# Performance work log

Hardware: AMD Instinct MI355X
Metric: run time of the kernel (lower is better)

Reference implementation:

```python
import jax, jax.numpy as jnp
import numpy as np

P = 7    # output_size (7,7)
SR = 2   # sampling_ratio per bin (torchvision roi_align samples per bin)


def _roi_avg_pool(feature_map, rois):
    """Fused roi_align(output_size=PxP) + adaptive_avg_pool2d(1,1).

    Since every bin averages SR*SR equally-weighted samples and the global
    average pool then averages the P*P bins, the result equals the mean over
    all P*SR x P*SR bilinear samples -- the 7x7 grid is never materialized.
    """
    B, C, H, W = feature_map.shape
    bidx = rois[:, 0].astype(jnp.int32)                       # [N]
    # get_anns: fp32 math, stored into an fp16 tensor (replicate the rounding).
    # NOTE (faithful to source): x coords are scaled by H (shape[2]) and y by W.
    f16 = lambda v: v.astype(jnp.float16).astype(jnp.float32)
    x1 = f16((rois[:, 2] - 0.5 * rois[:, 4]) * H)
    y1 = f16((rois[:, 3] - 0.5 * rois[:, 5]) * W)
    x2 = f16((rois[:, 2] + 0.5 * rois[:, 4]) * H)
    y2 = f16((rois[:, 3] + 0.5 * rois[:, 5]) * W)

    # torchvision roi_align, spatial_scale=1, aligned=False
    roi_w = jnp.maximum(x2 - x1, 1.0)
    roi_h = jnp.maximum(y2 - y1, 1.0)
    # sample offsets: bin pw plus (ix+0.5)/SR within the bin, in units of bin size
    offs = (jnp.arange(P, dtype=jnp.float32)[:, None]
            + (jnp.arange(SR, dtype=jnp.float32)[None, :] + 0.5) / SR).reshape(-1)  # [P*SR]
    xs = x1[:, None] + offs[None, :] * (roi_w / P)[:, None]   # [N,S] along width
    ys = y1[:, None] + offs[None, :] * (roi_h / P)[:, None]   # [N,S] along height

    valid = (((ys > -1.0) & (ys < H))[:, :, None]
             & ((xs > -1.0) & (xs < W))[:, None, :])          # [N,S,S]
    yc = jnp.clip(ys, 0.0, H - 1.0)
    xc = jnp.clip(xs, 0.0, W - 1.0)
    y0 = jnp.floor(yc).astype(jnp.int32)
    x0 = jnp.floor(xc).astype(jnp.int32)
    y1i = jnp.minimum(y0 + 1, H - 1)
    x1i = jnp.minimum(x0 + 1, W - 1)
    ly = yc - y0
    lx = xc - x0
    hy = 1.0 - ly
    hx = 1.0 - lx

    feat_t = jnp.transpose(feature_map, (0, 2, 3, 1))         # [B,H,W,C]

    def gather(yy, xx):  # yy,xx: [N,S] -> [N,S,S,C]
        return feat_t[bidx[:, None, None], yy[:, :, None], xx[:, None, :]]

    w = lambda a, b: (a[:, :, None] * b[:, None, :])[..., None]
    val = (w(hy, hx) * gather(y0, x0) + w(hy, lx) * gather(y0, x1i)
           + w(ly, hx) * gather(y1i, x0) + w(ly, lx) * gather(y1i, x1i))
    val = jnp.where(valid[..., None], val, 0.0)
    return val.mean(axis=(1, 2))                              # [N,C]


def setup_inputs() -> dict:
    key = jax.random.key(0)
    k1, k2, k3, k4 = jax.random.split(key, 4)
    B, C, H, W, N = 4, 256, 128, 128, 512
    feature_map = jax.random.normal(k1, (B, C, H, W), dtype=jnp.float32)
    # sorted batch indices so the original per-batch regrouping keeps ROI order
    bidx = jnp.sort(jax.random.randint(k2, (N,), 0, B)).astype(jnp.float32)
    cls = jax.random.randint(k3, (N,), 0, 20).astype(jnp.float32)
    kc, kw = jax.random.split(k4)
    cxcy = jax.random.uniform(kc, (N, 2), minval=0.2, maxval=0.8, dtype=jnp.float32)
    wh = jax.random.uniform(kw, (N, 2), minval=0.05, maxval=0.4, dtype=jnp.float32)
    rois = jnp.concatenate([bidx[:, None], cls[:, None], cxcy, wh], axis=1)  # [N,6]
    return {"feature_map": feature_map, "rois": rois}


def reference(feature_map, rois):
    roi_feats = _roi_avg_pool(feature_map, rois)   # [N, C] (original returns len-N list of [1,C])
    gt = rois[:, 1]                                # class labels
    return roi_feats, gt
```

## Files before the change

### kernel.cpp

```cpp
#include <hip/hip_runtime.h>
#include <hip/hip_fp16.h>
#include <hip/hip_bf16.h>

#define PP 7
#define SR 2
#define HH 128
#define WW 128
#define CC 256
#define PLANE (HH * WW)
#define MAXB 8
#define SLOT_BYTES 32768
#define WY_BASE (8 * SLOT_BYTES)
#define TAB_OFF (2 * WY_BASE)

typedef unsigned int uint;
typedef short bf16x8 __attribute__((ext_vector_type(8)));
typedef float f32x16 __attribute__((ext_vector_type(16)));

typedef const __attribute__((address_space(1))) void g_void;
typedef __attribute__((address_space(3))) void l_void;

__device__ __forceinline__ void gload_lds16(const void* g, void* lds_base) {
  __builtin_amdgcn_global_load_lds((g_void*)g, (l_void*)lds_base, 16, 0, 0);
}

__device__ __forceinline__ uint pkbf(float a, float b) {
  __hip_bfloat16 ha = __float2bfloat16(a), hb = __float2bfloat16(b);
  return (uint)*(unsigned short*)&ha | ((uint)*(unsigned short*)&hb << 16);
}

__global__ __launch_bounds__(64) void setup_kernel(
    const float* __restrict__ rois, unsigned char* wsb, int N, int B) {
  __shared__ int c[MAXB];
  const int t = threadIdx.x;
  if (t < MAXB) c[t] = 0;
  __syncthreads();
  for (int j = t; j < N; j += 64) atomicAdd(&c[(int)rois[j * 6]], 1);
  __syncthreads();
  if (t == 0) {
    int* tab = (int*)(wsb + TAB_OFF);
    int s = 0, tb = 0;
    for (int i = 0; i < B; ++i) {
      tab[i] = s; tab[24 + i] = c[i];
      const int tc = (c[i] + 127) >> 7;
      tab[8 + i] = tc; tab[16 + i] = tb;
      s += c[i]; tb += tc;
    }
  }
}

__global__ __launch_bounds__(64) void roi_meta_kernel(
    const float* __restrict__ rois, unsigned char* wsb,
    float* __restrict__ out, int N) {
  const int roi = blockIdx.x;
  const int lane = threadIdx.x;

  __shared__ float WXs[WW], WYs[HH];
  WXs[lane] = 0.f; WXs[lane + 64] = 0.f;
  WYs[lane] = 0.f; WYs[lane + 64] = 0.f;
  __syncthreads();

  const float bf = rois[roi * 6 + 0];
  const float cx = rois[roi * 6 + 2];
  const float cy = rois[roi * 6 + 3];
  const float w_ = rois[roi * 6 + 4];
  const float h_ = rois[roi * 6 + 5];

  const float x1 = __half2float(__float2half(
      __fmul_rn(__fsub_rn(cx, __fmul_rn(0.5f, w_)), 128.0f)));
  const float y1 = __half2float(__float2half(
      __fmul_rn(__fsub_rn(cy, __fmul_rn(0.5f, h_)), 128.0f)));
  const float x2 = __half2float(__float2half(
      __fmul_rn(__fadd_rn(cx, __fmul_rn(0.5f, w_)), 128.0f)));
  const float y2 = __half2float(__float2half(
      __fmul_rn(__fadd_rn(cy, __fmul_rn(0.5f, h_)), 128.0f)));

  const float sx = fmaxf(__fsub_rn(x2, x1), 1.0f) / 7.0f;
  const float sy = fmaxf(__fsub_rn(y2, y1), 1.0f) / 7.0f;

  if (lane < 2 * PP * SR) {
    const int isX = lane >= PP * SR;
    const int i = lane - isX * PP * SR;
    const float off = (float)(i >> 1) + ((float)(i & 1) + 0.5f) * 0.5f;
    const float pos = __fadd_rn(isX ? x1 : y1, __fmul_rn(off, isX ? sx : sy));
    if (pos > -1.0f && pos < 128.0f) {
      const float pc = fminf(fmaxf(pos, 0.0f), 127.0f);
      const int p0 = (int)floorf(pc);
      const int p1 = min(p0 + 1, 127);
      const float l = pc - (float)p0;
      float* Warr = isX ? WXs : WYs;
      atomicAdd(&Warr[p0], 1.0f - l);
      atomicAdd(&Warr[p1], l);
    }
  }
  __syncthreads();

  const int* tab = (const int*)(wsb + TAB_OFF);
  const int img = (int)bf;
  const int rl = roi - tab[img];
  const int slot = tab[16 + img] + (rl >> 7);
  const int col = rl & 127;

  const int sw = ((((lane >> 2) ^ (col & 7)) << 4) | ((lane & 3) << 2));
  *(uint*)(wsb + (size_t)slot * SLOT_BYTES + col * 256 + sw) =
      pkbf(WXs[2 * lane], WXs[2 * lane + 1]);
  __hip_bfloat16 h0 = __float2bfloat16(WYs[lane]);
  __hip_bfloat16 h1 = __float2bfloat16(WYs[lane + 64]);
  unsigned char* wyb = wsb + WY_BASE + (size_t)slot * SLOT_BYTES + col * 2;
  *(unsigned short*)(wyb + lane * 256) = *(unsigned short*)&h0;
  *(unsigned short*)(wyb + (lane + 64) * 256) = *(unsigned short*)&h1;

  if (lane == 0) out[(size_t)N * CC + roi] = rois[roi * 6 + 1];
}

__global__ __launch_bounds__(256, 2) void roi_gemm_kernel(
    const float* __restrict__ fm, const unsigned char* __restrict__ wsb,
    float* __restrict__ out, int N) {
  const int bid = blockIdx.x;
  const int ch = bid & (CC - 1);
  const int img = bid >> 8;
  const int t = threadIdx.x, wave = t >> 6, lane = t & 63;

  const int* tab = (const int*)(wsb + TAB_OFF);
  const int tcnt = tab[8 + img];
  if (tcnt == 0) return;
  const int istart = tab[img], Rimg = tab[24 + img], tbase = tab[16 + img];

  __shared__ unsigned char A[32768];
  __shared__ unsigned char BXl[32768];
  __shared__ float partial[4][128];

  const float* pb = fm + ((size_t)img * CC + ch) * PLANE;
  #pragma unroll
  for (int k = 0; k < 8; ++k) {
    const int cid = k * 256 + t;
    const float4 v0 = *(const float4*)(pb + (size_t)cid * 8);
    const float4 v1 = *(const float4*)(pb + (size_t)cid * 8 + 4);
    const int row = cid >> 4, x8 = cid & 15;
    const int boff = (row << 8) | ((x8 ^ (row & 7)) << 4);
    uint4 u;
    u.x = pkbf(v0.x, v0.y); u.y = pkbf(v0.z, v0.w);
    u.z = pkbf(v1.x, v1.y); u.w = pkbf(v1.z, v1.w);
    *(uint4*)(A + boff) = u;
  }

  const int m0 = wave * 32;
  const int arow = m0 + (lane & 31);
  const int ar7 = arow & 7;
  const unsigned char* Arow = A + (arow << 8);
  const int ahalf = lane >> 5;
  const int r7 = lane & 7;

  for (int ti = 0; ti < tcnt; ++ti) {
    const unsigned char* BXg = wsb + (size_t)(tbase + ti) * SLOT_BYTES;
    const unsigned char* BY = wsb + WY_BASE + (size_t)(tbase + ti) * SLOT_BYTES;

    #pragma unroll
    for (int k2 = 0; k2 < 8; ++k2)
      gload_lds16(BXg + k2 * 4096 + wave * 1024 + (lane << 4),
                  BXl + k2 * 4096 + wave * 1024);
    asm volatile("s_waitcnt vmcnt(0)" ::: "memory");
    __syncthreads();

    f32x16 ac0 = {}, ac1 = {}, ac2 = {}, ac3 = {};

    auto ldA = [&](int ks) -> bf16x8 {
      const int idx = (ahalf + 2 * ks) ^ ar7;
      return *(const bf16x8*)(Arow + (idx << 4));
    };
    auto ldB = [&](int ks, int ni) -> bf16x8 {
      const int c = (2 * ks + ahalf) ^ r7;
      return *(const bf16x8*)(BXl + (((lane & 31) + 32 * ni) << 8) + (c << 4));
    };

    bf16x8 a = ldA(0);
    bf16x8 b0 = ldB(0, 0), b1 = ldB(0, 1), b2 = ldB(0, 2), b3 = ldB(0, 3);
    #pragma unroll
    for (int ks = 0; ks < 8; ++ks) {
      bf16x8 an{}, bn0{}, bn1{}, bn2{}, bn3{};
      if (ks < 7) {
        an = ldA(ks + 1);
        bn0 = ldB(ks + 1, 0); bn1 = ldB(ks + 1, 1);
        bn2 = ldB(ks + 1, 2); bn3 = ldB(ks + 1, 3);
      }
      ac0 = __builtin_amdgcn_mfma_f32_32x32x16_bf16(a, b0, ac0, 0, 0, 0);
      ac1 = __builtin_amdgcn_mfma_f32_32x32x16_bf16(a, b1, ac1, 0, 0, 0);
      ac2 = __builtin_amdgcn_mfma_f32_32x32x16_bf16(a, b2, ac2, 0, 0, 0);
      ac3 = __builtin_amdgcn_mfma_f32_32x32x16_bf16(a, b3, ac3, 0, 0, 0);
      a = an; b0 = bn0; b1 = bn1; b2 = bn2; b3 = bn3;
    }

    #pragma unroll
    for (int ni = 0; ni < 4; ++ni) {
      const f32x16 acc = ni == 0 ? ac0 : ni == 1 ? ac1 : ni == 2 ? ac2 : ac3;
      float p = 0.f;
      #pragma unroll
      for (int j = 0; j < 16; ++j) {
        const int y = m0 + (j & 3) + 8 * (j >> 2) + 4 * ahalf;
        const unsigned short wy =
            *(const unsigned short*)(BY + y * 256 + (ni * 32 + (lane & 31)) * 2);
        p = fmaf(__uint_as_float((uint)wy << 16), acc[j], p);
      }
      p += __shfl_xor(p, 32, 64);
      if (lane < 32) partial[wave][ni * 32 + lane] = p;
    }
    __syncthreads();
    if (t < 128) {
      const int rl = ti * 128 + t;
      if (rl < Rimg) {
        const float s = partial[0][t] + partial[1][t] + partial[2][t] + partial[3][t];
        out[(size_t)(istart + rl) * CC + ch] = s * (1.0f / 196.0f);
      }
    }
    __syncthreads();
  }
}

extern "C" void kernel_launch(void* const* d_in, const int* in_sizes, int n_in,
                              void* d_out, int out_size, void* d_ws, size_t ws_size,
                              hipStream_t stream) {
  const float* fm   = (const float*)d_in[0];
  const float* rois = (const float*)d_in[1];
  float* out = (float*)d_out;
  unsigned char* wsb = (unsigned char*)d_ws;
  const int N = in_sizes[1] / 6;
  const int B = in_sizes[0] / (CC * PLANE);
  setup_kernel<<<1, 64, 0, stream>>>(rois, wsb, N, B);
  roi_meta_kernel<<<N, 64, 0, stream>>>(rois, wsb, out, N);
  roi_gemm_kernel<<<B * CC, 256, 0, stream>>>(fm, wsb, out, N);
}
```

Before: 31.79 us.

## Keep feature-plane A fragments in registers instead of LDS, raise occupancy

The bf16-converted feature plane is now loaded straight from global memory into per-lane registers (8 uint4 per lane), in MFMA fragment layout, rather than staged through a 32KB LDS buffer. The A loads overlap the first B-tile global-to-LDS transfer. Halving LDS use per block allows the launch bound to rise from 2 to 4 blocks per CU, improving latency hiding. The explicit software prefetch of LDS operands is dropped and scheduling is left to the compiler. Register pressure rises and the per-lane global reads are less coalesced (32-byte chunks per row).

```diff
diff --git a/kernel.cpp b/kernel.cpp
--- a/kernel.cpp
+++ b/kernel.cpp
@@ -113,7 +113,7 @@
   if (lane == 0) out[(size_t)N * CC + roi] = rois[roi * 6 + 1];
 }
 
-__global__ __launch_bounds__(256, 2) void roi_gemm_kernel(
+__global__ __launch_bounds__(256, 4) void roi_gemm_kernel(
     const float* __restrict__ fm, const unsigned char* __restrict__ wsb,
     float* __restrict__ out, int N) {
   const int bid = blockIdx.x;
@@ -126,30 +126,16 @@
   if (tcnt == 0) return;
   const int istart = tab[img], Rimg = tab[24 + img], tbase = tab[16 + img];
 
-  __shared__ unsigned char A[32768];
   __shared__ unsigned char BXl[32768];
   __shared__ float partial[4][128];
 
-  const float* pb = fm + ((size_t)img * CC + ch) * PLANE;
-  #pragma unroll
-  for (int k = 0; k < 8; ++k) {
-    const int cid = k * 256 + t;
-    const float4 v0 = *(const float4*)(pb + (size_t)cid * 8);
-    const float4 v1 = *(const float4*)(pb + (size_t)cid * 8 + 4);
-    const int row = cid >> 4, x8 = cid & 15;
-    const int boff = (row << 8) | ((x8 ^ (row & 7)) << 4);
-    uint4 u;
-    u.x = pkbf(v0.x, v0.y); u.y = pkbf(v0.z, v0.w);
-    u.z = pkbf(v1.x, v1.y); u.w = pkbf(v1.z, v1.w);
-    *(uint4*)(A + boff) = u;
-  }
-
   const int m0 = wave * 32;
   const int arow = m0 + (lane & 31);
-  const int ar7 = arow & 7;
-  const unsigned char* Arow = A + (arow << 8);
   const int ahalf = lane >> 5;
   const int r7 = lane & 7;
+
+  const float* pb = fm + ((size_t)img * CC + ch) * PLANE;
+  uint4 a[8];
 
   for (int ti = 0; ti < tcnt; ++ti) {
     const unsigned char* BXg = wsb + (size_t)(tbase + ti) * SLOT_BYTES;
@@ -159,35 +145,36 @@
     for (int k2 = 0; k2 < 8; ++k2)
       gload_lds16(BXg + k2 * 4096 + wave * 1024 + (lane << 4),
                   BXl + k2 * 4096 + wave * 1024);
+
+    if (ti == 0) {
+      const float* prow = pb + arow * WW + 8 * ahalf;
+      #pragma unroll
+      for (int ks = 0; ks < 8; ++ks) {
+        const float4 u0 = *(const float4*)(prow + 16 * ks);
+        const float4 u1 = *(const float4*)(prow + 16 * ks + 4);
+        uint4 P;
+        P.x = pkbf(u0.x, u0.y); P.y = pkbf(u0.z, u0.w);
+        P.z = pkbf(u1.x, u1.y); P.w = pkbf(u1.z, u1.w);
+        a[ks] = P;
+      }
+    }
     asm volatile("s_waitcnt vmcnt(0)" ::: "memory");
     __syncthreads();
 
     f32x16 ac0 = {}, ac1 = {}, ac2 = {}, ac3 = {};
 
-    auto ldA = [&](int ks) -> bf16x8 {
-      const int idx = (ahalf + 2 * ks) ^ ar7;
-      return *(const bf16x8*)(Arow + (idx << 4));
-    };
     auto ldB = [&](int ks, int ni) -> bf16x8 {
       const int c = (2 * ks + ahalf) ^ r7;
       return *(const bf16x8*)(BXl + (((lane & 31) + 32 * ni) << 8) + (c << 4));
     };
 
-    bf16x8 a = ldA(0);
-    bf16x8 b0 = ldB(0, 0), b1 = ldB(0, 1), b2 = ldB(0, 2), b3 = ldB(0, 3);
     #pragma unroll
     for (int ks = 0; ks < 8; ++ks) {
-      bf16x8 an{}, bn0{}, bn1{}, bn2{}, bn3{};
-      if (ks < 7) {
-        an = ldA(ks + 1);
-        bn0 = ldB(ks + 1, 0); bn1 = ldB(ks + 1, 1);
-        bn2 = ldB(ks + 1, 2); bn3 = ldB(ks + 1, 3);
-      }
-      ac0 = __builtin_amdgcn_mfma_f32_32x32x16_bf16(a, b0, ac0, 0, 0, 0);
-      ac1 = __builtin_amdgcn_mfma_f32_32x32x16_bf16(a, b1, ac1, 0, 0, 0);
-      ac2 = __builtin_amdgcn_mfma_f32_32x32x16_bf16(a, b2, ac2, 0, 0, 0);
-      ac3 = __builtin_amdgcn_mfma_f32_32x32x16_bf16(a, b3, ac3, 0, 0, 0);
-      a = an; b0 = bn0; b1 = bn1; b2 = bn2; b3 = bn3;
+      const bf16x8 av = __builtin_bit_cast(bf16x8, a[ks]);
+      ac0 = __builtin_amdgcn_mfma_f32_32x32x16_bf16(av, ldB(ks, 0), ac0, 0, 0, 0);
+      ac1 = __builtin_amdgcn_mfma_f32_32x32x16_bf16(av, ldB(ks, 1), ac1, 0, 0, 0);
+      ac2 = __builtin_amdgcn_mfma_f32_32x32x16_bf16(av, ldB(ks, 2), ac2, 0, 0, 0);
+      ac3 = __builtin_amdgcn_mfma_f32_32x32x16_bf16(av, ldB(ks, 3), ac3, 0, 0, 0);
     }
 
     #pragma unroll
```

Result: slower. 49.22 us (+54.8%).

## Drop setup kernel, binary-search ROI ranges, pipeline 4 channels per block

Applied to the files above, without the earlier changes.

Removes the single-block setup kernel. Each consumer now finds per-image ROI start offsets by binary search over the sorted batch indices, which saves one launch and one serial dependency. The GEMM kernel now handles 4 channels per block instead of 1 and loads up to two ROI weight tiles into LDS once for all of them. It double-buffers the feature plane loads in registers so the global fetch of the next channel overlaps the convert and MFMA work of the current one. The costs are fewer blocks (B*64), occupancy lowered to 1 block per CU, and heavy register use for the prefetch buffers.

```diff
diff --git a/kernel.cpp b/kernel.cpp
--- a/kernel.cpp
+++ b/kernel.cpp
@@ -8,10 +8,8 @@
 #define WW 128
 #define CC 256
 #define PLANE (HH * WW)
-#define MAXB 8
 #define SLOT_BYTES 32768
 #define WY_BASE (8 * SLOT_BYTES)
-#define TAB_OFF (2 * WY_BASE)
 
 typedef unsigned int uint;
 typedef short bf16x8 __attribute__((ext_vector_type(8)));
@@ -29,35 +27,27 @@
   return (uint)*(unsigned short*)&ha | ((uint)*(unsigned short*)&hb << 16);
 }
 
-__global__ __launch_bounds__(64) void setup_kernel(
-    const float* __restrict__ rois, unsigned char* wsb, int N, int B) {
-  __shared__ int c[MAXB];
-  const int t = threadIdx.x;
-  if (t < MAXB) c[t] = 0;
-  __syncthreads();
-  for (int j = t; j < N; j += 64) atomicAdd(&c[(int)rois[j * 6]], 1);
-  __syncthreads();
-  if (t == 0) {
-    int* tab = (int*)(wsb + TAB_OFF);
-    int s = 0, tb = 0;
-    for (int i = 0; i < B; ++i) {
-      tab[i] = s; tab[24 + i] = c[i];
-      const int tc = (c[i] + 127) >> 7;
-      tab[8 + i] = tc; tab[16 + i] = tb;
-      s += c[i]; tb += tc;
-    }
+__device__ __forceinline__ int lb_img(const float* rois, int N, float v) {
+  int lo = 0, hi = N;
+  while (lo < hi) {
+    const int mid = (lo + hi) >> 1;
+    if (rois[mid * 6] < v) lo = mid + 1; else hi = mid;
   }
+  return lo;
 }
 
 __global__ __launch_bounds__(64) void roi_meta_kernel(
     const float* __restrict__ rois, unsigned char* wsb,
-    float* __restrict__ out, int N) {
+    float* __restrict__ out, int N, int B) {
   const int roi = blockIdx.x;
   const int lane = threadIdx.x;
 
   __shared__ float WXs[WW], WYs[HH];
   WXs[lane] = 0.f; WXs[lane + 64] = 0.f;
   WYs[lane] = 0.f; WYs[lane + 64] = 0.f;
+
+  int lbv = 0;
+  if (lane <= B) lbv = lb_img(rois, N, (float)lane);
   __syncthreads();
 
   const float bf = rois[roi * 6 + 0];
@@ -95,10 +85,13 @@
   }
   __syncthreads();
 
-  const int* tab = (const int*)(wsb + TAB_OFF);
   const int img = (int)bf;
-  const int rl = roi - tab[img];
-  const int slot = tab[16 + img] + (rl >> 7);
+  const int myStart = __shfl(lbv, img, 64);
+  int tb = 0;
+  for (int i = 0; i < img; ++i)
+    tb += (__shfl(lbv, i + 1, 64) - __shfl(lbv, i, 64) + 127) >> 7;
+  const int rl = roi - myStart;
+  const int slot = tb + (rl >> 7);
   const int col = rl & 127;
 
   const int sw = ((((lane >> 2) ^ (col & 7)) << 4) | ((lane & 3) << 2));
@@ -113,37 +106,51 @@
   if (lane == 0) out[(size_t)N * CC + roi] = rois[roi * 6 + 1];
 }
 
-__global__ __launch_bounds__(256, 2) void roi_gemm_kernel(
-    const float* __restrict__ fm, const unsigned char* __restrict__ wsb,
-    float* __restrict__ out, int N) {
+#define ISSUE_PLANE(u, cc) do { \
+  const float* pb_ = pimg + (size_t)(c0 + (cc)) * PLANE; \
+  _Pragma("unroll") \
+  for (int k_ = 0; k_ < 8; ++k_) { \
+    const int cid_ = k_ * 256 + t; \
+    u[2*k_]   = *(const float4*)(pb_ + (size_t)cid_ * 8); \
+    u[2*k_+1] = *(const float4*)(pb_ + (size_t)cid_ * 8 + 4); \
+  } } while (0)
+
+#define CONVERT_PLANE(u) do { \
+  _Pragma("unroll") \
+  for (int k_ = 0; k_ < 8; ++k_) { \
+    const int cid_ = k_ * 256 + t; \
+    const int row_ = cid_ >> 4, x8_ = cid_ & 15; \
+    const int boff_ = (row_ << 8) | ((x8_ ^ (row_ & 7)) << 4); \
+    uint4 P_; \
+    P_.x = pkbf(u[2*k_].x, u[2*k_].y);     P_.y = pkbf(u[2*k_].z, u[2*k_].w); \
+    P_.z = pkbf(u[2*k_+1].x, u[2*k_+1].y); P_.w = pkbf(u[2*k_+1].z, u[2*k_+1].w); \
+    *(uint4*)(A + boff_) = P_; \
+  } } while (0)
+
+__global__ __launch_bounds__(256, 1) void roi_gemm_kernel(
+    const float* __restrict__ fm, const float* __restrict__ rois,
+    const unsigned char* __restrict__ wsb, float* __restrict__ out,
+    int N, int B) {
   const int bid = blockIdx.x;
-  const int ch = bid & (CC - 1);
-  const int img = bid >> 8;
+  const int img = bid >> 6;
+  const int c0 = (bid & 63) * 4;
   const int t = threadIdx.x, wave = t >> 6, lane = t & 63;
 
-  const int* tab = (const int*)(wsb + TAB_OFF);
-  const int tcnt = tab[8 + img];
-  if (tcnt == 0) return;
-  const int istart = tab[img], Rimg = tab[24 + img], tbase = tab[16 + img];
-
   __shared__ unsigned char A[32768];
-  __shared__ unsigned char BXl[32768];
+  __shared__ unsigned char BXl[2][32768];
   __shared__ float partial[4][128];
 
-  const float* pb = fm + ((size_t)img * CC + ch) * PLANE;
-  #pragma unroll
-  for (int k = 0; k < 8; ++k) {
-    const int cid = k * 256 + t;
-    const float4 v0 = *(const float4*)(pb + (size_t)cid * 8);
-    const float4 v1 = *(const float4*)(pb + (size_t)cid * 8 + 4);
-    const int row = cid >> 4, x8 = cid & 15;
-    const int boff = (row << 8) | ((x8 ^ (row & 7)) << 4);
-    uint4 u;
-    u.x = pkbf(v0.x, v0.y); u.y = pkbf(v0.z, v0.w);
-    u.z = pkbf(v1.x, v1.y); u.w = pkbf(v1.z, v1.w);
-    *(uint4*)(A + boff) = u;
-  }
-
+  int lbv = 0;
+  if (lane <= B) lbv = lb_img(rois, N, (float)lane);
+  const int istart = __shfl(lbv, img, 64);
+  const int cnt = __shfl(lbv, img + 1, 64) - istart;
+  if (cnt == 0) return;
+  int tbase = 0;
+  for (int i = 0; i < img; ++i)
+    tbase += (__shfl(lbv, i + 1, 64) - __shfl(lbv, i, 64) + 127) >> 7;
+  const int tcnt = (cnt + 127) >> 7;
+
+  const float* pimg = fm + (size_t)img * CC * PLANE;
   const int m0 = wave * 32;
   const int arow = m0 + (lane & 31);
   const int ar7 = arow & 7;
@@ -151,68 +158,91 @@
   const int ahalf = lane >> 5;
   const int r7 = lane & 7;
 
-  for (int ti = 0; ti < tcnt; ++ti) {
-    const unsigned char* BXg = wsb + (size_t)(tbase + ti) * SLOT_BYTES;
-    const unsigned char* BY = wsb + WY_BASE + (size_t)(tbase + ti) * SLOT_BYTES;
+  float4 uA[16], uB[16];
+
+  for (int tp = 0; tp < ((tcnt + 1) >> 1); ++tp) {
+    const int t0 = tp * 2;
+    const int ntile = min(2, tcnt - t0);
+
+    for (int b_ = 0; b_ < ntile; ++b_) {
+      const unsigned char* BXg = wsb + (size_t)(tbase + t0 + b_) * SLOT_BYTES;
+      #pragma unroll
+      for (int k2 = 0; k2 < 8; ++k2)
+        gload_lds16(BXg + k2 * 4096 + wave * 1024 + (lane << 4),
+                    &BXl[b_][0] + k2 * 4096 + wave * 1024);
+    }
+    ISSUE_PLANE(uA, 0);
 
     #pragma unroll
-    for (int k2 = 0; k2 < 8; ++k2)
-      gload_lds16(BXg + k2 * 4096 + wave * 1024 + (lane << 4),
-                  BXl + k2 * 4096 + wave * 1024);
-    asm volatile("s_waitcnt vmcnt(0)" ::: "memory");
-    __syncthreads();
-
-    f32x16 ac0 = {}, ac1 = {}, ac2 = {}, ac3 = {};
-
-    auto ldA = [&](int ks) -> bf16x8 {
-      const int idx = (ahalf + 2 * ks) ^ ar7;
-      return *(const bf16x8*)(Arow + (idx << 4));
-    };
-    auto ldB = [&](int ks, int ni) -> bf16x8 {
-      const int c = (2 * ks + ahalf) ^ r7;
-      return *(const bf16x8*)(BXl + (((lane & 31) + 32 * ni) << 8) + (c << 4));
-    };
-
-    bf16x8 a = ldA(0);
-    bf16x8 b0 = ldB(0, 0), b1 = ldB(0, 1), b2 = ldB(0, 2), b3 = ldB(0, 3);
-    #pragma unroll
-    for (int ks = 0; ks < 8; ++ks) {
-      bf16x8 an{}, bn0{}, bn1{}, bn2{}, bn3{};
-      if (ks < 7) {
-        an = ldA(ks + 1);
-        bn0 = ldB(ks + 1, 0); bn1 = ldB(ks + 1, 1);
-        bn2 = ldB(ks + 1, 2); bn3 = ldB(ks + 1, 3);
-      }
-      ac0 = __builtin_amdgcn_mfma_f32_32x32x16_bf16(a, b0, ac0, 0, 0, 0);
-      ac1 = __builtin_amdgcn_mfma_f32_32x32x16_bf16(a, b1, ac1, 0, 0, 0);
-      ac2 = __builtin_amdgcn_mfma_f32_32x32x16_bf16(a, b2, ac2, 0, 0, 0);
-      ac3 = __builtin_amdgcn_mfma_f32_32x32x16_bf16(a, b3, ac3, 0, 0, 0);
-      a = an; b0 = bn0; b1 = bn1; b2 = bn2; b3 = bn3;
-    }
-
-    #pragma unroll
-    for (int ni = 0; ni < 4; ++ni) {
-      const f32x16 acc = ni == 0 ? ac0 : ni == 1 ? ac1 : ni == 2 ? ac2 : ac3;
-      float p = 0.f;
-      #pragma unroll
-      for (int j = 0; j < 16; ++j) {
-        const int y = m0 + (j & 3) + 8 * (j >> 2) + 4 * ahalf;
-        const unsigned short wy =
-            *(const unsigned short*)(BY + y * 256 + (ni * 32 + (lane & 31)) * 2);
-        p = fmaf(__uint_as_float((uint)wy << 16), acc[j], p);
-      }
-      p += __shfl_xor(p, 32, 64);
-      if (lane < 32) partial[wave][ni * 32 + lane] = p;
-    }
-    __syncthreads();
-    if (t < 128) {
-      const int rl = ti * 128 + t;
-      if (rl < Rimg) {
-        const float s = partial[0][t] + partial[1][t] + partial[2][t] + partial[3][t];
-        out[(size_t)(istart + rl) * CC + ch] = s * (1.0f / 196.0f);
+    for (int c = 0; c < 4; ++c) {
+      if (c == 0)      ISSUE_PLANE(uB, 1);
+      else if (c == 1) ISSUE_PLANE(uA, 2);
+      else if (c == 2) ISSUE_PLANE(uB, 3);
+      if (c < 3) asm volatile("s_waitcnt vmcnt(16)" ::: "memory");
+      else       asm volatile("s_waitcnt vmcnt(0)" ::: "memory");
+      __builtin_amdgcn_sched_barrier(0);
+      if (c & 1) CONVERT_PLANE(uB); else CONVERT_PLANE(uA);
+      __syncthreads();
+
+      for (int ti = 0; ti < ntile; ++ti) {
+        const unsigned char* BY =
+            wsb + WY_BASE + (size_t)(tbase + t0 + ti) * SLOT_BYTES;
+
+        f32x16 ac0 = {}, ac1 = {}, ac2 = {}, ac3 = {};
+
+        auto ldA = [&](int ks) -> bf16x8 {
+          const int idx = (ahalf + 2 * ks) ^ ar7;
+          return *(const bf16x8*)(Arow + (idx << 4));
+        };
+        auto ldB = [&](int ks, int ni) -> bf16x8 {
+          const int csw = (2 * ks + ahalf) ^ r7;
+          return *(const bf16x8*)(&BXl[ti][0] +
+                                  (((lane & 31) + 32 * ni) << 8) + (csw << 4));
+        };
+
+        bf16x8 a = ldA(0);
+        bf16x8 b0 = ldB(0, 0), b1 = ldB(0, 1), b2 = ldB(0, 2), b3 = ldB(0, 3);
+        #pragma unroll
+        for (int ks = 0; ks < 8; ++ks) {
+          bf16x8 an{}, bn0{}, bn1{}, bn2{}, bn3{};
+          if (ks < 7) {
+            an = ldA(ks + 1);
+            bn0 = ldB(ks + 1, 0); bn1 = ldB(ks + 1, 1);
+            bn2 = ldB(ks + 1, 2); bn3 = ldB(ks + 1, 3);
+          }
+          ac0 = __builtin_amdgcn_mfma_f32_32x32x16_bf16(a, b0, ac0, 0, 0, 0);
+          ac1 = __builtin_amdgcn_mfma_f32_32x32x16_bf16(a, b1, ac1, 0, 0, 0);
+          ac2 = __builtin_amdgcn_mfma_f32_32x32x16_bf16(a, b2, ac2, 0, 0, 0);
+          ac3 = __builtin_amdgcn_mfma_f32_32x32x16_bf16(a, b3, ac3, 0, 0, 0);
+          a = an; b0 = bn0; b1 = bn1; b2 = bn2; b3 = bn3;
+        }
+
+        #pragma unroll
+        for (int ni = 0; ni < 4; ++ni) {
+          const f32x16 acc = ni == 0 ? ac0 : ni == 1 ? ac1 : ni == 2 ? ac2 : ac3;
+          float p = 0.f;
+          #pragma unroll
+          for (int j = 0; j < 16; ++j) {
+            const int y = m0 + (j & 3) + 8 * (j >> 2) + 4 * ahalf;
+            const unsigned short wy = *(const unsigned short*)(
+                BY + y * 256 + (ni * 32 + (lane & 31)) * 2);
+            p = fmaf(__uint_as_float((uint)wy << 16), acc[j], p);
+          }
+          p += __shfl_xor(p, 32, 64);
+          if (lane < 32) partial[wave][ni * 32 + lane] = p;
+        }
+        __syncthreads();
+        if (t < 128) {
+          const int rl = (t0 + ti) * 128 + t;
+          if (rl < cnt) {
+            const float s =
+                partial[0][t] + partial[1][t] + partial[2][t] + partial[3][t];
+            out[(size_t)(istart + rl) * CC + (c0 + c)] = s * (1.0f / 196.0f);
+          }
+        }
+        __syncthreads();
       }
     }
-    __syncthreads();
   }
 }
 
@@ -225,7 +255,6 @@
   unsigned char* wsb = (unsigned char*)d_ws;
   const int N = in_sizes[1] / 6;
   const int B = in_sizes[0] / (CC * PLANE);
-  setup_kernel<<<1, 64, 0, stream>>>(rois, wsb, N, B);
-  roi_meta_kernel<<<N, 64, 0, stream>>>(rois, wsb, out, N);
-  roi_gemm_kernel<<<B * CC, 256, 0, stream>>>(fm, wsb, out, N);
-}
+  roi_meta_kernel<<<N, 64, 0, stream>>>(rois, wsb, out, N, B);
+  roi_gemm_kernel<<<B * 64, 256, 0, stream>>>(fm, rois, wsb, out, N, B);
+}
```

New measurement: 40.93 us. +28.8%, slower.
